# Optimization experiments

Measured on AMD Instinct MI355X. Metric: run time of the kernel, lower is better.

Reference implementation:

```python
import jax, jax.numpy as jnp
import numpy as np


def gcn_conv(x, edge_index, edge_weight, W, b):
    """PyG-style GCNConv: h = x @ W; add self-loops (w=1); sym deg^-1/2 norm;
    scatter-add aggregation; + bias."""
    N = x.shape[0]
    h = x @ W                                   # [N, F_out]
    row, col = edge_index[0], edge_index[1]     # src, dst
    loop = jnp.arange(N)
    row = jnp.concatenate([row, loop])
    col = jnp.concatenate([col, loop])
    ew = jnp.concatenate([edge_weight, jnp.ones((N,), edge_weight.dtype)])
    deg = jax.ops.segment_sum(ew, col, num_segments=N)
    dinv = jnp.where(deg > 0, deg ** -0.5, 0.0)
    norm = dinv[row] * ew * dinv[col]           # [E+N]
    out = jax.ops.segment_sum(h[row] * norm[:, None], col, num_segments=N)
    return out + b


def setup_inputs() -> dict:
    key = jax.random.key(0)
    ks = jax.random.split(key, 12)
    N, F_in, H, O, E = 20000, 3000, 512, 256, 640000
    x = jax.random.normal(ks[0], (N, F_in), dtype=jnp.float32)
    sim_edge_index = jax.random.randint(ks[1], (2, E), 0, N, dtype=jnp.int64)
    sim_edge_weight = jax.random.uniform(ks[2], (E,), dtype=jnp.float32)
    dist_edge_index = jax.random.randint(ks[3], (2, E), 0, N, dtype=jnp.int64)
    dist_edge_weight = jax.random.uniform(ks[4], (E,), dtype=jnp.float32)
    s = 0.02
    return {
        "x": x,
        "sim_edge_index": sim_edge_index,
        "sim_edge_weight": sim_edge_weight,
        "dist_edge_index": dist_edge_index,
        "dist_edge_weight": dist_edge_weight,
        "W1": jax.random.normal(ks[5], (F_in, H), dtype=jnp.float32) * s,
        "b1": jnp.zeros((H,), jnp.float32),
        "W2": jax.random.normal(ks[6], (F_in, H), dtype=jnp.float32) * s,
        "b2": jnp.zeros((H,), jnp.float32),
        "Ws": jax.random.normal(ks[7], (H, O), dtype=jnp.float32) * s,
        "bs": jnp.zeros((O,), jnp.float32),
        "Wd": jax.random.normal(ks[8], (H, O), dtype=jnp.float32) * s,
        "bd": jnp.zeros((O,), jnp.float32),
        "Wf": jax.random.normal(ks[9], (2 * O, O), dtype=jnp.float32) * s,
        "bf": jnp.zeros((O,), jnp.float32),
    }


def reference(x, sim_edge_index, sim_edge_weight, dist_edge_index,
              dist_edge_weight, W1, b1, W2, b2, Ws, bs, Wd, bd, Wf, bf):
    # eval mode: dropout is identity
    xs = jax.nn.relu(gcn_conv(x, sim_edge_index, sim_edge_weight, W1, b1))
    xd = jax.nn.relu(gcn_conv(x, dist_edge_index, dist_edge_weight, W2, b2))
    x_sim = gcn_conv(xs, sim_edge_index, sim_edge_weight, Ws, bs)
    x_dist = gcn_conv(xd, dist_edge_index, dist_edge_weight, Wd, bd)
    fused = jnp.concatenate([x_sim, x_dist], axis=1) @ Wf + bf
    return (x_sim, x_dist, fused)
```

## Files before the change

### kernel.cpp

```cpp
#include <hip/hip_runtime.h>
#include <cstdint>
#include <cstddef>

typedef unsigned short u16;
typedef __bf16 bf16x8 __attribute__((ext_vector_type(8)));
typedef float f32x4 __attribute__((ext_vector_type(4)));

#define N_NODES 20000
#define MPAD    20096
#define E_EDGES 640000
#define K1      3000
#define K1P     3008
#define H_DIM   512
#define NW      1024
#define O_DIM   256

__device__ __forceinline__ float bf2f(unsigned int hi) {
  union { unsigned int u; float f; } v; v.u = hi << 16; return v.f;
}
__device__ __forceinline__ u16 f2bf(float f) {
  union { float f; unsigned int u; } v; v.f = f;
  unsigned int u = v.u;
  return (u16)((u + 0x7fffu + ((u >> 16) & 1u)) >> 16);
}

__device__ __forceinline__ void gl2lds16(const void* g, void* l) {
  __builtin_amdgcn_global_load_lds((const __attribute__((address_space(1))) void*)g,
                                   (__attribute__((address_space(3))) void*)l, 16, 0, 0);
}

__global__ __launch_bounds__(256) void deg_init_k(float* degS, float* degD, int* cntS, int* cntD) {
  int i = blockIdx.x * 256 + threadIdx.x;
  if (i < N_NODES) { degS[i] = 1.0f; degD[i] = 1.0f; cntS[i] = 0; cntD[i] = 0; }
}

__global__ __launch_bounds__(256) void deg_accum_k(const int* eiS, const float* ewS,
                                                   const int* eiD, const float* ewD,
                                                   float* degS, float* degD, int* cntS, int* cntD) {
  int e = blockIdx.x * 256 + threadIdx.x;
  if (e < E_EDGES) {
    int cs = eiS[E_EDGES + e];
    atomicAdd(&degS[cs], ewS[e]);
    atomicAdd(&cntS[cs], 1);
    int cd = eiD[E_EDGES + e];
    atomicAdd(&degD[cd], ewD[e]);
    atomicAdd(&cntD[cd], 1);
  }
}

__global__ __launch_bounds__(256) void dinv_k(const float* degS, const float* degD,
                                              float* dinvS, float* dinvD) {
  int i = blockIdx.x * 256 + threadIdx.x;
  if (i < N_NODES) { dinvS[i] = rsqrtf(degS[i]); dinvD[i] = rsqrtf(degD[i]); }
}

__global__ __launch_bounds__(1024) void scan_k(const int* cntS, int* offS, int* curS,
                                               const int* cntD, int* offD, int* curD) {
  const int* cnt = blockIdx.x ? cntD : cntS;
  int* off = blockIdx.x ? offD : offS;
  int* cur = blockIdx.x ? curD : curS;
  __shared__ int sums[1024];
  const int t = threadIdx.x;
  const int CH = 20;
  int base = t * CH;
  int s = 0;
  for (int j = 0; j < CH; ++j) { int idx = base + j; if (idx < N_NODES) s += cnt[idx]; }
  sums[t] = s;
  __syncthreads();
  for (int d = 1; d < 1024; d <<= 1) {
    int v = (t >= d) ? sums[t - d] : 0;
    __syncthreads();
    sums[t] += v;
    __syncthreads();
  }
  int run = sums[t] - s;
  for (int j = 0; j < CH; ++j) {
    int idx = base + j;
    if (idx <= N_NODES) {
      off[idx] = run; cur[idx] = run;
      if (idx < N_NODES) run += cnt[idx];
    }
  }
}

__global__ __launch_bounds__(256) void scatter_k(const int* eiS, const float* ewS, const float* dinvS,
                                                 int* curS, int* ssrcS, float* snrmS,
                                                 const int* eiD, const float* ewD, const float* dinvD,
                                                 int* curD, int* ssrcD, float* snrmD) {
  int e = blockIdx.x * 256 + threadIdx.x;
  if (e < E_EDGES) {
    {
      int r = eiS[e], c = eiS[E_EDGES + e];
      int pos = atomicAdd(&curS[c], 1);
      ssrcS[pos] = r;
      snrmS[pos] = dinvS[r] * ewS[e] * dinvS[c];
    }
    {
      int r = eiD[e], c = eiD[E_EDGES + e];
      int pos = atomicAdd(&curD[c], 1);
      ssrcD[pos] = r;
      snrmD[pos] = dinvD[r] * ewD[e] * dinvD[c];
    }
  }
}

__global__ __launch_bounds__(256) void conv_w12_k(const float* __restrict__ W1,
                                                  const float* __restrict__ W2,
                                                  u16* __restrict__ w12t) {
  __shared__ float t[64][65];
  const int kb = blockIdx.x;
  const int nb = blockIdx.y;
  const int n0 = nb * 64;
  const float* W = (n0 < H_DIM) ? W1 : W2;
  const int nn0 = n0 & (H_DIM - 1);
  const int k0 = kb * 64;
  const int tc = threadIdx.x & 63;
  const int tr4 = threadIdx.x >> 6;
#pragma unroll
  for (int rr = 0; rr < 16; ++rr) {
    int r = tr4 * 16 + rr;
    int k = k0 + r;
    t[r][tc] = (k < K1) ? W[(size_t)k * H_DIM + nn0 + tc] : 0.f;
  }
  __syncthreads();
#pragma unroll
  for (int rr = 0; rr < 16; ++rr) {
    int n = tr4 * 16 + rr;
    w12t[(size_t)(n0 + n) * K1P + k0 + tc] = f2bf(t[tc][n]);
  }
}

__global__ __launch_bounds__(256) void conv_wsm_k(const float* Ws, const float* Wd, const float* Wf,
                                                  u16* wst, u16* wdt, u16* wft) {
  __shared__ float t[64][65];
  const int which = blockIdx.z;
  const float* W = (which == 0) ? Ws : (which == 1) ? Wd : Wf;
  u16* o = (which == 0) ? wst : (which == 1) ? wdt : wft;
  const int k0 = blockIdx.x * 64;
  const int n0 = blockIdx.y * 64;
  const int tc = threadIdx.x & 63;
  const int tr4 = threadIdx.x >> 6;
#pragma unroll
  for (int rr = 0; rr < 16; ++rr) {
    int r = tr4 * 16 + rr;
    t[r][tc] = W[(size_t)(k0 + r) * O_DIM + n0 + tc];
  }
  __syncthreads();
#pragma unroll
  for (int rr = 0; rr < 16; ++rr) {
    int n = tr4 * 16 + rr;
    o[(size_t)(n0 + n) * H_DIM + k0 + tc] = f2bf(t[tc][n]);
  }
}

template <typename CT, bool BIAS>
__device__ __forceinline__ void gemm_body(const u16* __restrict__ A, const u16* __restrict__ Bt,
                                          CT* __restrict__ C, const float* __restrict__ bias,
                                          int Mreal, int K, int ldc) {
  __shared__ alignas(16) u16 As[128 * 64];
  __shared__ alignas(16) u16 Bs[128 * 64];
  const int tid = threadIdx.x;
  const int lane = tid & 63;
  const int wv = tid >> 6;
  const int bm = blockIdx.y * 128;
  const int bn = blockIdx.x * 128;

  const int wm = (wv >> 1) << 6;
  const int wn = (wv & 1) << 6;
  const int frow = lane & 15;
  const int q = lane >> 4;
  const int r7 = lane & 7;

  const int srow = tid >> 3;
  const int sgr = ((tid & 7) ^ ((tid >> 3) & 7)) << 3;
  const u16* ga = A + (size_t)(bm + srow) * K + sgr;
  const u16* gb = Bt + (size_t)(bn + srow) * K + sgr;
  u16* la = &As[wv * 512];
  u16* lb = &Bs[wv * 512];

  f32x4 acc[4][4] = {};

  for (int k0 = 0; k0 < K; k0 += 64) {
#pragma unroll
    for (int r = 0; r < 4; ++r) {
      gl2lds16(ga + (size_t)(r * 32) * K + k0, la + r * 2048);
      gl2lds16(gb + (size_t)(r * 32) * K + k0, lb + r * 2048);
    }
    __syncthreads();
#pragma unroll
    for (int ks = 0; ks < 64; ks += 32) {
      const int p = (((q + (ks >> 3)) ^ r7) << 3);
      bf16x8 af[4], bv[4];
#pragma unroll
      for (int t = 0; t < 4; ++t) {
        af[t] = *(const bf16x8*)&As[(wm + t * 16 + frow) * 64 + p];
        bv[t] = *(const bf16x8*)&Bs[(wn + t * 16 + frow) * 64 + p];
      }
#pragma unroll
      for (int i = 0; i < 4; ++i)
#pragma unroll
        for (int j = 0; j < 4; ++j)
          acc[i][j] = __builtin_amdgcn_mfma_f32_16x16x32_bf16(af[i], bv[j], acc[i][j], 0, 0, 0);
    }
    __syncthreads();
  }

  const int crow = (lane >> 4) << 2;
  const int ccol = lane & 15;
#pragma unroll
  for (int i = 0; i < 4; ++i) {
#pragma unroll
    for (int r = 0; r < 4; ++r) {
      int gr = bm + wm + i * 16 + crow + r;
      if (gr < Mreal) {
#pragma unroll
        for (int j = 0; j < 4; ++j) {
          int gc = bn + wn + j * 16 + ccol;
          float v = acc[i][j][r];
          if constexpr (BIAS) v += bias[gc];
          if constexpr (sizeof(CT) == 2) C[(size_t)gr * ldc + gc] = (CT)f2bf(v);
          else C[(size_t)gr * ldc + gc] = (CT)v;
        }
      }
    }
  }
}

__global__ __launch_bounds__(256) void gemm_pair_k(const u16* A0, const u16* B0, u16* C0,
                                                   const u16* A1, const u16* B1, u16* C1) {
  const u16* A = blockIdx.z ? A1 : A0;
  const u16* Bt = blockIdx.z ? B1 : B0;
  u16* C = blockIdx.z ? C1 : C0;
  gemm_body<u16, false>(A, Bt, C, nullptr, N_NODES, H_DIM, O_DIM);
}

__global__ __launch_bounds__(256) void gemm_f_k(const u16* A, const u16* Bt, float* C,
                                                const float* bias) {
  gemm_body<float, true>(A, Bt, C, bias, N_NODES, H_DIM, O_DIM);
}

__global__ __launch_bounds__(256) void gemm_x_k(const float* __restrict__ X,
                                                const u16* __restrict__ Bt,
                                                u16* __restrict__ C) {
  __shared__ alignas(16) u16 As[128 * 64];
  __shared__ alignas(16) u16 Bs[128 * 64];
  const int tid = threadIdx.x;
  const int lane = tid & 63;
  const int wv = tid >> 6;

  const int h = blockIdx.y * 8 + blockIdx.x;
  const int chunk = 157;
  const int L = (h & 7) * chunk + (h >> 3);
  const int bn = (L & 7) * 128;
  const int bm = (L >> 3) * 128;

  const int wm = (wv >> 1) << 6;
  const int wn = (wv & 1) << 6;
  const int frow = lane & 15;
  const int q = lane >> 4;
  const int r7 = lane & 7;

  const int srow = tid >> 3;
  const int lgr = (tid & 7) ^ (srow & 7);
  const float* xa[4];
#pragma unroll
  for (int r = 0; r < 4; ++r) {
    int row = bm + srow + r * 32;
    if (row >= N_NODES) row = 0;
    xa[r] = X + (size_t)row * K1 + lgr * 8;
  }
  const u16* gb = Bt + (size_t)(bn + srow) * K1P + (lgr << 3);
  u16* lb = &Bs[wv * 512];

  f32x4 acc[4][4] = {};

  for (int k0 = 0; k0 < K1P; k0 += 64) {
#pragma unroll
    for (int r = 0; r < 4; ++r)
      gl2lds16(gb + (size_t)(r * 32) * K1P + k0, lb + r * 2048);
#pragma unroll
    for (int r = 0; r < 4; ++r) {
      float4 v0 = *(const float4*)(xa[r] + k0);
      float4 v1 = *(const float4*)(xa[r] + k0 + 4);
      bf16x8 pk;
      pk[0] = (__bf16)v0.x; pk[1] = (__bf16)v0.y; pk[2] = (__bf16)v0.z; pk[3] = (__bf16)v0.w;
      pk[4] = (__bf16)v1.x; pk[5] = (__bf16)v1.y; pk[6] = (__bf16)v1.z; pk[7] = (__bf16)v1.w;
      *(bf16x8*)&As[r * 2048 + tid * 8] = pk;
    }
    __syncthreads();
#pragma unroll
    for (int ks = 0; ks < 64; ks += 32) {
      const int p = (((q + (ks >> 3)) ^ r7) << 3);
      bf16x8 af[4], bv[4];
#pragma unroll
      for (int t = 0; t < 4; ++t) {
        af[t] = *(const bf16x8*)&As[(wm + t * 16 + frow) * 64 + p];
        bv[t] = *(const bf16x8*)&Bs[(wn + t * 16 + frow) * 64 + p];
      }
#pragma unroll
      for (int i = 0; i < 4; ++i)
#pragma unroll
        for (int j = 0; j < 4; ++j)
          acc[i][j] = __builtin_amdgcn_mfma_f32_16x16x32_bf16(af[i], bv[j], acc[i][j], 0, 0, 0);
    }
    __syncthreads();
  }

  const int crow = (lane >> 4) << 2;
  const int ccol = lane & 15;
#pragma unroll
  for (int i = 0; i < 4; ++i) {
#pragma unroll
    for (int r = 0; r < 4; ++r) {
      int gr = bm + wm + i * 16 + crow + r;
      if (gr < N_NODES) {
#pragma unroll
        for (int j = 0; j < 4; ++j) {
          int gc = bn + wn + j * 16 + ccol;
          C[(size_t)gr * NW + gc] = f2bf(acc[i][j][r]);
        }
      }
    }
  }
}

__global__ __launch_bounds__(256) void agg1_k(const u16* __restrict__ h12,
                                              const int* offS, const int* srcS, const float* nrmS,
                                              const float* dinvS, const float* b1,
                                              const int* offD, const int* srcD, const float* nrmD,
                                              const float* dinvD, const float* b2,
                                              u16* __restrict__ xsd) {
  const int lane = threadIdx.x & 63;
  const int wv = threadIdx.x >> 6;
  const int i = blockIdx.x * 4 + wv;
  const int g = blockIdx.y;
  if (i >= MPAD) return;
  u16* outp = xsd + ((size_t)g * MPAD + i) * H_DIM + lane * 8;
  if (i >= N_NODES) { uint4 z = {0, 0, 0, 0}; *(uint4*)outp = z; return; }

  const int* off = g ? offD : offS;
  const int* src = g ? srcD : srcS;
  const float* nrm = g ? nrmD : nrmS;
  const float* dinv = g ? dinvD : dinvS;
  const float* bias = g ? b2 : b1;
  const u16* hb = h12 + (size_t)g * H_DIM + lane * 8;

  float a[8];
  float dv = dinv[i];
  float sw = dv * dv;
  uint4 u = *(const uint4*)(hb + (size_t)i * NW);
  a[0] = sw * bf2f(u.x & 0xffff); a[1] = sw * bf2f(u.x >> 16);
  a[2] = sw * bf2f(u.y & 0xffff); a[3] = sw * bf2f(u.y >> 16);
  a[4] = sw * bf2f(u.z & 0xffff); a[5] = sw * bf2f(u.z >> 16);
  a[6] = sw * bf2f(u.w & 0xffff); a[7] = sw * bf2f(u.w >> 16);

  const int e0 = off[i], e1 = off[i + 1];
  int e = e0;
  for (; e + 4 <= e1; e += 4) {
    int ss[4]; float ww[4];
#pragma unroll
    for (int t = 0; t < 4; ++t) { ss[t] = src[e + t]; ww[t] = nrm[e + t]; }
    uint4 vv[4];
#pragma unroll
    for (int t = 0; t < 4; ++t) vv[t] = *(const uint4*)(hb + (size_t)ss[t] * NW);
#pragma unroll
    for (int t = 0; t < 4; ++t) {
      float w = ww[t]; uint4 v = vv[t];
      a[0] += w * bf2f(v.x & 0xffff); a[1] += w * bf2f(v.x >> 16);
      a[2] += w * bf2f(v.y & 0xffff); a[3] += w * bf2f(v.y >> 16);
      a[4] += w * bf2f(v.z & 0xffff); a[5] += w * bf2f(v.z >> 16);
      a[6] += w * bf2f(v.w & 0xffff); a[7] += w * bf2f(v.w >> 16);
    }
  }
  for (; e < e1; ++e) {
    int s = src[e];
    float w = nrm[e];
    uint4 v = *(const uint4*)(hb + (size_t)s * NW);
    a[0] += w * bf2f(v.x & 0xffff); a[1] += w * bf2f(v.x >> 16);
    a[2] += w * bf2f(v.y & 0xffff); a[3] += w * bf2f(v.y >> 16);
    a[4] += w * bf2f(v.z & 0xffff); a[5] += w * bf2f(v.z >> 16);
    a[6] += w * bf2f(v.w & 0xffff); a[7] += w * bf2f(v.w >> 16);
  }
  float4 bA = *(const float4*)(bias + lane * 8);
  float4 bB = *(const float4*)(bias + lane * 8 + 4);
  a[0] = fmaxf(a[0] + bA.x, 0.f); a[1] = fmaxf(a[1] + bA.y, 0.f);
  a[2] = fmaxf(a[2] + bA.z, 0.f); a[3] = fmaxf(a[3] + bA.w, 0.f);
  a[4] = fmaxf(a[4] + bB.x, 0.f); a[5] = fmaxf(a[5] + bB.y, 0.f);
  a[6] = fmaxf(a[6] + bB.z, 0.f); a[7] = fmaxf(a[7] + bB.w, 0.f);
  uint4 o;
  o.x = f2bf(a[0]) | ((unsigned)f2bf(a[1]) << 16);
  o.y = f2bf(a[2]) | ((unsigned)f2bf(a[3]) << 16);
  o.z = f2bf(a[4]) | ((unsigned)f2bf(a[5]) << 16);
  o.w = f2bf(a[6]) | ((unsigned)f2bf(a[7]) << 16);
  *(uint4*)outp = o;
}

__global__ __launch_bounds__(256) void agg2_k(const u16* __restrict__ hsb, const u16* __restrict__ hdb,
                                              const int* offS, const int* srcS, const float* nrmS,
                                              const float* dinvS, const float* bs,
                                              const int* offD, const int* srcD, const float* nrmD,
                                              const float* dinvD, const float* bd,
                                              float* __restrict__ outF, u16* __restrict__ xcat) {
  const int lane = threadIdx.x & 63;
  const int wv = threadIdx.x >> 6;
  const int i = blockIdx.x * 4 + wv;
  const int g = blockIdx.y;
  if (i >= MPAD) return;
  u16* oc = xcat + (size_t)i * H_DIM + (size_t)g * O_DIM + lane * 4;
  if (i >= N_NODES) { uint2 z = {0, 0}; *(uint2*)oc = z; return; }

  const u16* h = g ? hdb : hsb;
  const int* off = g ? offD : offS;
  const int* src = g ? srcD : srcS;
  const float* nrm = g ? nrmD : nrmS;
  const float* dinv = g ? dinvD : dinvS;
  const float* bias = g ? bd : bs;
  const u16* hb = h + lane * 4;

  float a[4];
  float dv = dinv[i];
  float sw = dv * dv;
  uint2 u = *(const uint2*)(hb + (size_t)i * O_DIM);
  a[0] = sw * bf2f(u.x & 0xffff); a[1] = sw * bf2f(u.x >> 16);
  a[2] = sw * bf2f(u.y & 0xffff); a[3] = sw * bf2f(u.y >> 16);

  const int e0 = off[i], e1 = off[i + 1];
  int e = e0;
  for (; e + 8 <= e1; e += 8) {
    int ss[8]; float ww[8];
#pragma unroll
    for (int t = 0; t < 8; ++t) { ss[t] = src[e + t]; ww[t] = nrm[e + t]; }
    uint2 vv[8];
#pragma unroll
    for (int t = 0; t < 8; ++t) vv[t] = *(const uint2*)(hb + (size_t)ss[t] * O_DIM);
#pragma unroll
    for (int t = 0; t < 8; ++t) {
      float w = ww[t]; uint2 v = vv[t];
      a[0] += w * bf2f(v.x & 0xffff); a[1] += w * bf2f(v.x >> 16);
      a[2] += w * bf2f(v.y & 0xffff); a[3] += w * bf2f(v.y >> 16);
    }
  }
  for (; e < e1; ++e) {
    int s = src[e];
    float w = nrm[e];
    uint2 v = *(const uint2*)(hb + (size_t)s * O_DIM);
    a[0] += w * bf2f(v.x & 0xffff); a[1] += w * bf2f(v.x >> 16);
    a[2] += w * bf2f(v.y & 0xffff); a[3] += w * bf2f(v.y >> 16);
  }
  float4 bb = *(const float4*)(bias + lane * 4);
  a[0] += bb.x; a[1] += bb.y; a[2] += bb.z; a[3] += bb.w;

  float4 fo = {a[0], a[1], a[2], a[3]};
  *(float4*)(outF + (size_t)g * N_NODES * O_DIM + (size_t)i * O_DIM + lane * 4) = fo;
  uint2 o;
  o.x = f2bf(a[0]) | ((unsigned)f2bf(a[1]) << 16);
  o.y = f2bf(a[2]) | ((unsigned)f2bf(a[3]) << 16);
  *(uint2*)oc = o;
}

extern "C" void kernel_launch(void* const* d_in, const int* in_sizes, int n_in,
                              void* d_out, int out_size, void* d_ws, size_t ws_size,
                              hipStream_t stream) {
  const float* x = (const float*)d_in[0];
  const int* eiS = (const int*)d_in[1];
  const float* ewS = (const float*)d_in[2];
  const int* eiD = (const int*)d_in[3];
  const float* ewD = (const float*)d_in[4];
  const float* W1 = (const float*)d_in[5];
  const float* b1 = (const float*)d_in[6];
  const float* W2 = (const float*)d_in[7];
  const float* b2 = (const float*)d_in[8];
  const float* Ws = (const float*)d_in[9];
  const float* bs = (const float*)d_in[10];
  const float* Wd = (const float*)d_in[11];
  const float* bd = (const float*)d_in[12];
  const float* Wf = (const float*)d_in[13];
  const float* bf_ = (const float*)d_in[14];
  float* out = (float*)d_out;

  char* p = (char*)d_ws;
  auto alloc = [&](size_t n) -> char* { char* r = p; p += (n + 255) & ~(size_t)255; return r; };

  u16* w12t  = (u16*)alloc((size_t)NW * K1P * 2);
  u16* h12   = (u16*)alloc((size_t)N_NODES * NW * 2);
  u16* xsd   = (u16*)alloc((size_t)2 * MPAD * H_DIM * 2);
  u16* hsb   = (u16*)alloc((size_t)N_NODES * O_DIM * 2);
  u16* hdb   = (u16*)alloc((size_t)N_NODES * O_DIM * 2);
  u16* xcat  = (u16*)alloc((size_t)MPAD * H_DIM * 2);
  u16* wst   = (u16*)alloc((size_t)O_DIM * H_DIM * 2);
  u16* wdt   = (u16*)alloc((size_t)O_DIM * H_DIM * 2);
  u16* wft   = (u16*)alloc((size_t)O_DIM * H_DIM * 2);
  float* degS = (float*)alloc((size_t)N_NODES * 4);
  float* degD = (float*)alloc((size_t)N_NODES * 4);
  float* dinvS = (float*)alloc((size_t)N_NODES * 4);
  float* dinvD = (float*)alloc((size_t)N_NODES * 4);
  int* cntS = (int*)alloc((size_t)N_NODES * 4);
  int* cntD = (int*)alloc((size_t)N_NODES * 4);
  int* offS = (int*)alloc((size_t)(N_NODES + 1) * 4);
  int* offD = (int*)alloc((size_t)(N_NODES + 1) * 4);
  int* curS = (int*)alloc((size_t)(N_NODES + 1) * 4);
  int* curD = (int*)alloc((size_t)(N_NODES + 1) * 4);
  int* ssrcS = (int*)alloc((size_t)E_EDGES * 4);
  int* ssrcD = (int*)alloc((size_t)E_EDGES * 4);
  float* snrmS = (float*)alloc((size_t)E_EDGES * 4);
  float* snrmD = (float*)alloc((size_t)E_EDGES * 4);

  const int gN = (N_NODES + 255) / 256;
  const int gE = (E_EDGES + 255) / 256;

  deg_init_k<<<gN, 256, 0, stream>>>(degS, degD, cntS, cntD);
  deg_accum_k<<<gE, 256, 0, stream>>>(eiS, ewS, eiD, ewD, degS, degD, cntS, cntD);
  dinv_k<<<gN, 256, 0, stream>>>(degS, degD, dinvS, dinvD);
  scan_k<<<2, 1024, 0, stream>>>(cntS, offS, curS, cntD, offD, curD);
  scatter_k<<<gE, 256, 0, stream>>>(eiS, ewS, dinvS, curS, ssrcS, snrmS,
                                    eiD, ewD, dinvD, curD, ssrcD, snrmD);

  conv_w12_k<<<dim3(47, 16), 256, 0, stream>>>(W1, W2, w12t);
  conv_wsm_k<<<dim3(8, 4, 3), 256, 0, stream>>>(Ws, Wd, Wf, wst, wdt, wft);

  gemm_x_k<<<dim3(8, 157), 256, 0, stream>>>(x, w12t, h12);

  agg1_k<<<dim3(MPAD / 4, 2), 256, 0, stream>>>(h12, offS, ssrcS, snrmS, dinvS, b1,
                                                offD, ssrcD, snrmD, dinvD, b2, xsd);

  gemm_pair_k<<<dim3(2, 157, 2), 256, 0, stream>>>(xsd, wst, hsb,
                                                   xsd + (size_t)MPAD * H_DIM, wdt, hdb);

  agg2_k<<<dim3(MPAD / 4, 2), 256, 0, stream>>>(hsb, hdb, offS, ssrcS, snrmS, dinvS, bs,
                                                offD, ssrcD, snrmD, dinvD, bd, out, xcat);

  gemm_f_k<<<dim3(2, 157), 256, 0, stream>>>(xcat, wft, out + (size_t)2 * N_NODES * O_DIM, bf_);
}
```

Before: 1.078 ms.

## Double-buffer LDS tiles in the x@W GEMM to overlap loads with MFMA

Splits the A and B shared-memory tiles into two buffers in the fp32-input GEMM kernel. The next K tile is prefetched while MFMAs run on the current one: B through direct global-to-LDS copies, and A as fp32 register loads that are converted to bf16 and stored after the compute. This removes one barrier per iteration and hides global-load latency. In exchange it doubles LDS use to 64KB per block, which can lower occupancy, and raises register pressure. The final tile's out-of-range X reads are redirected to offset 0 and land against zero-padded B columns.

```diff
diff --git a/kernel.cpp b/kernel.cpp
--- a/kernel.cpp
+++ b/kernel.cpp
@@ -242,8 +242,8 @@
 __global__ __launch_bounds__(256) void gemm_x_k(const float* __restrict__ X,
                                                 const u16* __restrict__ Bt,
                                                 u16* __restrict__ C) {
-  __shared__ alignas(16) u16 As[128 * 64];
-  __shared__ alignas(16) u16 Bs[128 * 64];
+  __shared__ alignas(16) u16 As[2][128 * 64];
+  __shared__ alignas(16) u16 Bs[2][128 * 64];
   const int tid = threadIdx.x;
   const int lane = tid & 63;
   const int wv = tid >> 6;
@@ -270,32 +270,56 @@
     xa[r] = X + (size_t)row * K1 + lgr * 8;
   }
   const u16* gb = Bt + (size_t)(bn + srow) * K1P + (lgr << 3);
-  u16* lb = &Bs[wv * 512];
 
   f32x4 acc[4][4] = {};
-
-  for (int k0 = 0; k0 < K1P; k0 += 64) {
+  constexpr int NT = K1P / 64;
+
+  {
+    float4 a0[4], a1[4];
+#pragma unroll
+    for (int r = 0; r < 4; ++r) {
+      a0[r] = *(const float4*)(xa[r]);
+      a1[r] = *(const float4*)(xa[r] + 4);
+    }
 #pragma unroll
     for (int r = 0; r < 4; ++r)
-      gl2lds16(gb + (size_t)(r * 32) * K1P + k0, lb + r * 2048);
+      gl2lds16(gb + (size_t)(r * 32) * K1P, &Bs[0][wv * 512] + r * 2048);
 #pragma unroll
     for (int r = 0; r < 4; ++r) {
-      float4 v0 = *(const float4*)(xa[r] + k0);
-      float4 v1 = *(const float4*)(xa[r] + k0 + 4);
       bf16x8 pk;
-      pk[0] = (__bf16)v0.x; pk[1] = (__bf16)v0.y; pk[2] = (__bf16)v0.z; pk[3] = (__bf16)v0.w;
-      pk[4] = (__bf16)v1.x; pk[5] = (__bf16)v1.y; pk[6] = (__bf16)v1.z; pk[7] = (__bf16)v1.w;
-      *(bf16x8*)&As[r * 2048 + tid * 8] = pk;
+      pk[0] = (__bf16)a0[r].x; pk[1] = (__bf16)a0[r].y; pk[2] = (__bf16)a0[r].z; pk[3] = (__bf16)a0[r].w;
+      pk[4] = (__bf16)a1[r].x; pk[5] = (__bf16)a1[r].y; pk[6] = (__bf16)a1[r].z; pk[7] = (__bf16)a1[r].w;
+      *(bf16x8*)&As[0][r * 2048 + tid * 8] = pk;
     }
     __syncthreads();
+  }
+
+  int cur = 0;
+  for (int t = 0; t < NT; ++t) {
+    const int nxt = cur ^ 1;
+    float4 a0[4], a1[4];
+    const bool pf = (t + 1 < NT);
+    if (pf) {
+      int k0n = (t + 1) * 64;
+      if (k0n + (lgr << 3) >= K1) k0n = 0;
+#pragma unroll
+      for (int r = 0; r < 4; ++r) {
+        a0[r] = *(const float4*)(xa[r] + k0n);
+        a1[r] = *(const float4*)(xa[r] + k0n + 4);
+      }
+      const int k0b = (t + 1) * 64;
+#pragma unroll
+      for (int r = 0; r < 4; ++r)
+        gl2lds16(gb + (size_t)(r * 32) * K1P + k0b, &Bs[nxt][wv * 512] + r * 2048);
+    }
 #pragma unroll
     for (int ks = 0; ks < 64; ks += 32) {
       const int p = (((q + (ks >> 3)) ^ r7) << 3);
       bf16x8 af[4], bv[4];
 #pragma unroll
-      for (int t = 0; t < 4; ++t) {
-        af[t] = *(const bf16x8*)&As[(wm + t * 16 + frow) * 64 + p];
-        bv[t] = *(const bf16x8*)&Bs[(wn + t * 16 + frow) * 64 + p];
+      for (int u = 0; u < 4; ++u) {
+        af[u] = *(const bf16x8*)&As[cur][(wm + u * 16 + frow) * 64 + p];
+        bv[u] = *(const bf16x8*)&Bs[cur][(wn + u * 16 + frow) * 64 + p];
       }
 #pragma unroll
       for (int i = 0; i < 4; ++i)
@@ -303,7 +327,17 @@
         for (int j = 0; j < 4; ++j)
           acc[i][j] = __builtin_amdgcn_mfma_f32_16x16x32_bf16(af[i], bv[j], acc[i][j], 0, 0, 0);
     }
+    if (pf) {
+#pragma unroll
+      for (int r = 0; r < 4; ++r) {
+        bf16x8 pk;
+        pk[0] = (__bf16)a0[r].x; pk[1] = (__bf16)a0[r].y; pk[2] = (__bf16)a0[r].z; pk[3] = (__bf16)a0[r].w;
+        pk[4] = (__bf16)a1[r].x; pk[5] = (__bf16)a1[r].y; pk[6] = (__bf16)a1[r].z; pk[7] = (__bf16)a1[r].w;
+        *(bf16x8*)&As[nxt][r * 2048 + tid * 8] = pk;
+      }
+    }
     __syncthreads();
+    cur = nxt;
   }
 
   const int crow = (lane >> 4) << 2;
```

Result: slower. 1.182 ms (+9.6%).
